# Kernel tuning notes

Hardware: AMD Instinct MI355X
Metric: run time of the kernel (lower is better)

## Reference

```python
import jax, jax.numpy as jnp
import numpy as np

KSIZE = 7
FEAT_SIZE = 64
BETA = 0.02


def _resize_bilinear_ac(x, out_h, out_w):
    """Bilinear resize with align_corners=True. x: (B, C, H, W)."""
    H, W = x.shape[-2], x.shape[-1]
    ys = jnp.linspace(0.0, H - 1.0, out_h)
    xs = jnp.linspace(0.0, W - 1.0, out_w)
    y0 = jnp.clip(jnp.floor(ys).astype(jnp.int32), 0, H - 1)
    x0 = jnp.clip(jnp.floor(xs).astype(jnp.int32), 0, W - 1)
    y1 = jnp.minimum(y0 + 1, H - 1)
    x1 = jnp.minimum(x0 + 1, W - 1)
    wy = (ys - y0.astype(x.dtype))[None, None, :, None]
    wx = (xs - x0.astype(x.dtype))[None, None, None, :]
    rows = x[:, :, y0, :] * (1.0 - wy) + x[:, :, y1, :] * wy      # (B,C,out_h,W)
    out = rows[:, :, :, x0] * (1.0 - wx) + rows[:, :, :, x1] * wx  # (B,C,out_h,out_w)
    return out


def _sce(feat, w, b):
    """EfficientSpatialContextNet: shifted local-correlation context + 1x1 conv + relu."""
    B, C, h, wd = feat.shape
    k, pad = KSIZE, KSIZE // 2
    # F.normalize(p=2, dim=1) with eps=1e-12 (clamped norm)
    fn = feat / jnp.maximum(jnp.sqrt(jnp.sum(feat * feat, axis=1, keepdims=True)), 1e-12)
    fp = jnp.pad(fn, ((0, 0), (0, 0), (pad, pad), (pad, pad)))
    offsets = ([(i, i) for i in range(k)]
               + [(i, pad) for i in range(k)]
               + [(i, k - 1 - i) for i in range(k)]
               + [(pad, i) for i in range(k)])
    ctx = jnp.stack([jnp.sum(fp[:, :, r:h + r, c:wd + c] * fn, axis=1)
                     for (r, c) in offsets], axis=1)  # (B, 4k, h, w)
    out = jnp.concatenate([feat, ctx], axis=1)        # (B, C+4k, h, w)
    out = jnp.einsum('oc,bchw->bohw', w, out) + b[None, :, None, None]
    return jax.nn.relu(out)


def _l2norm(f):
    # FeatureL2Norm: eps added inside sqrt
    return f / jnp.sqrt(jnp.sum(f * f, axis=1, keepdims=True) + 1e-6)


def _forward(src_feat, tgt_feat, sce_w, sce_b):
    fs = FEAT_SIZE
    s = _l2norm(_sce(src_feat, sce_w, sce_b))
    t = _l2norm(_sce(tgt_feat, sce_w, sce_b))
    B, C, hs, ws = s.shape
    ht, wt = t.shape[2], t.shape[3]
    Ls, Lt = hs * ws, ht * wt
    corr = jnp.einsum('bcs,bct->bst', s.reshape(B, C, Ls), t.reshape(B, C, Lt))
    # mutual NN filter (Rocco et al.)
    smax = jnp.max(corr, axis=2, keepdims=True)
    tmax = jnp.max(corr, axis=1, keepdims=True)
    smax = jnp.where(smax == 0, 1e-30, smax)
    tmax = jnp.where(tmax == 0, 1e-30, tmax)
    corr = corr * ((corr / smax) * (corr / tmax))
    # resize corr on source grid, then on target grid (bilinear, align_corners=True)
    c_s2t = jnp.transpose(corr, (0, 2, 1)).reshape(B, Lt, hs, ws)
    c_s2t = _resize_bilinear_ac(c_s2t, fs, fs)                       # (B, Lt, fs, fs)
    c_t2s = jnp.transpose(c_s2t.reshape(B, Lt, fs * fs), (0, 2, 1)).reshape(B, fs * fs, ht, wt)
    c = _resize_bilinear_ac(c_t2s, fs, fs)                           # (B, fs*fs, fs, fs)
    # soft argmax with temperature (softmax over source positions)
    p = jax.nn.softmax(c / BETA, axis=1).reshape(B, fs, fs, fs, fs)  # (B, hs', ws', ht', wt')
    xn = jnp.linspace(-1.0, 1.0, fs).astype(c.dtype)
    yn = jnp.linspace(-1.0, 1.0, fs).astype(c.dtype)
    grid_x = jnp.einsum('bijhw,j->bhw', p, xn)
    grid_y = jnp.einsum('bijhw,i->bhw', p, yn)
    flow_norm = jnp.stack([grid_x, grid_y], axis=1)                  # (B, 2, fs, fs)
    # unnormalise mapping and convert to flow
    H = W = fs
    mx = (flow_norm[:, 0] + 1.0) * (W - 1) / 2.0
    my = (flow_norm[:, 1] + 1.0) * (H - 1) / 2.0
    xx = jnp.arange(W, dtype=flow_norm.dtype)[None, None, :]
    yy = jnp.arange(H, dtype=flow_norm.dtype)[None, :, None]
    flow = jnp.stack([mx - xx, my - yy], axis=1)                     # (B, 2, fs, fs)
    return flow


def setup_inputs() -> dict:
    key = jax.random.key(0)
    k1, k2, k3 = jax.random.split(key, 3)
    B, C, h, w = 4, 1024, 32, 32
    src_feat = jax.random.normal(k1, (B, C, h, w), dtype=jnp.float32)
    tgt_feat = jax.random.normal(k2, (B, C, h, w), dtype=jnp.float32)
    sce_w = jax.random.normal(k3, (2048, C + 4 * KSIZE), dtype=jnp.float32) * 0.03
    sce_b = jnp.zeros((2048,), dtype=jnp.float32)
    return {"src_feat": src_feat, "tgt_feat": tgt_feat, "sce_w": sce_w, "sce_b": sce_b}


def reference(src_feat, tgt_feat, sce_w, sce_b):
    return _forward(src_feat, tgt_feat, sce_w, sce_b)
```

## Files before the change

### kernel.cpp

```cpp
#include <hip/hip_runtime.h>
#include <math.h>

#define HW    1024
#define CIN   1024
#define CCTX  28
#define CALL  1052
#define COUT  2048
#define CCHNK 512

typedef _Float16 half8   __attribute__((ext_vector_type(8)));
typedef _Float16 half4_t __attribute__((ext_vector_type(4)));
typedef float    f32x4   __attribute__((ext_vector_type(4)));

__device__ __forceinline__ void split_f16(float x, _Float16& h, _Float16& l) {
    _Float16 hh = (_Float16)x;
    h = hh;
    l = (_Float16)(x - (float)hh);
}
__device__ __forceinline__ float f4get(const float4& v, int e) {
    return e == 0 ? v.x : e == 1 ? v.y : e == 2 ? v.z : v.w;
}

__global__ void pnorm_kernel(const float* __restrict__ src, const float* __restrict__ tgt,
                             float* __restrict__ pnorm) {
    int img = blockIdx.x;
    int p = blockIdx.y * 64 + threadIdx.x;
    const float* feat = (img < 4) ? src + (size_t)img * CIN * HW
                                  : tgt + (size_t)(img - 4) * CIN * HW;
    float ss = 0.f;
    for (int c = 0; c < CIN; ++c) {
        float v = feat[(size_t)c * HW + p];
        ss = fmaf(v, v, ss);
    }
    pnorm[img * HW + p] = fmaxf(sqrtf(ss), 1e-12f);
}

__global__ void ctx_kernel(const float* __restrict__ src, const float* __restrict__ tgt,
                           const float* __restrict__ pnorm, float* __restrict__ ctx) {
    int img = blockIdx.x;
    int y = blockIdx.y;
    int tid = threadIdx.x;
    int o = tid >> 5;
    int x = tid & 31;
    const float* feat = (img < 4) ? src + (size_t)img * CIN * HW
                                  : tgt + (size_t)(img - 4) * CIN * HW;
    int g = o / 7, i = o % 7;
    int r, c;
    if (g == 0)      { r = i; c = i; }
    else if (g == 1) { r = i; c = 3; }
    else if (g == 2) { r = i; c = 6 - i; }
    else             { r = 3; c = i; }
    int y2 = y + r - 3, x2 = x + c - 3;
    int p = y * 32 + x;
    float outv = 0.f;
    if (y2 >= 0 && y2 < 32 && x2 >= 0 && x2 < 32) {
        int p2 = y2 * 32 + x2;
        const float* f0 = feat + p;
        const float* f1 = feat + p2;
        float acc = 0.f;
        for (int ch = 0; ch < CIN; ++ch)
            acc = fmaf(f0[(size_t)ch * HW], f1[(size_t)ch * HW], acc);
        outv = acc / (pnorm[img * HW + p] * pnorm[img * HW + p2]);
    }
    ctx[((size_t)img * CCTX + o) * HW + p] = outv;
}

template <bool FIRST>
__global__ __launch_bounds__(256, 2) void conv_mfma(
    const float* __restrict__ src, const float* __restrict__ tgt,
    const float* __restrict__ ctxb, const float* __restrict__ w,
    const float* __restrict__ bias, float* __restrict__ ychunk,
    float* __restrict__ nrm_parts, int c0) {
    __shared__ __align__(16) char smem[55296];
    _Float16* Ah = (_Float16*)smem;
    _Float16* Al = Ah + 64 * 72;
    _Float16* Bh = Al + 64 * 72;
    _Float16* Bl = Bh + 128 * 72;

    int cb = blockIdx.x;
    int pb = blockIdx.y;
    int img = blockIdx.z;
    int n0 = pb * 64;
    int m0g = c0 + cb * 128;
    const float* feat = (img < 4) ? src + (size_t)img * CIN * HW
                                  : tgt + (size_t)(img - 4) * CIN * HW;
    const float* ctxi = ctxb + (size_t)img * CCTX * HW;
    int tid = threadIdx.x;

    int aq = tid & 15, ar = tid >> 4;
    int brow = tid >> 1, bh_ = tid & 1;

    float4 xa[4], xb[8];
    auto loadA = [&](int k0) {
#pragma unroll
        for (int j = 0; j < 4; ++j) {
            int k = k0 + ar * 4 + j;
            if (k < CIN)       xa[j] = *(const float4*)(feat + (size_t)k * HW + n0 + aq * 4);
            else if (k < CALL) xa[j] = *(const float4*)(ctxi + (size_t)(k - CIN) * HW + n0 + aq * 4);
            else               xa[j] = make_float4(0.f, 0.f, 0.f, 0.f);
        }
    };
    auto loadB = [&](int k0) {
#pragma unroll
        for (int i = 0; i < 8; ++i) {
            int k = k0 + bh_ * 32 + i * 4;
            xb[i] = (k < CALL) ? *(const float4*)(w + (size_t)(m0g + brow) * CALL + k)
                               : make_float4(0.f, 0.f, 0.f, 0.f);
        }
    };
    auto storeLDS = [&]() {
#pragma unroll
        for (int p = 0; p < 4; ++p) {
            half4_t h, l;
#pragma unroll
            for (int j = 0; j < 4; ++j) {
                _Float16 hh, ll; split_f16(f4get(xa[j], p), hh, ll);
                h[j] = hh; l[j] = ll;
            }
            int row = aq * 4 + p;
            *(half4_t*)(Ah + row * 72 + ar * 4) = h;
            *(half4_t*)(Al + row * 72 + ar * 4) = l;
        }
#pragma unroll
        for (int g = 0; g < 4; ++g) {
            half8 h, l;
#pragma unroll
            for (int e = 0; e < 8; ++e) {
                _Float16 hh, ll; split_f16(f4get(xb[g * 2 + (e >> 2)], e & 3), hh, ll);
                h[e] = hh; l[e] = ll;
            }
            *(half8*)(Bh + brow * 72 + bh_ * 32 + g * 8) = h;
            *(half8*)(Bl + brow * 72 + bh_ * 32 + g * 8) = l;
        }
    };

    int lane = tid & 63, wv = tid >> 6;
    int wm = wv >> 1, wn = wv & 1;
    int frow = lane & 15;
    int kcol = (lane >> 4) * 8;

    f32x4 acc[2][4] = {};
    const int NT = 17;
    loadA(0); loadB(0); storeLDS();
    __syncthreads();
    for (int s = 0; s < NT; ++s) {
        if (s + 1 < NT) { loadA((s + 1) * 64); loadB((s + 1) * 64); }
#pragma unroll
        for (int ks = 0; ks < 2; ++ks) {
            int ko = ks * 32 + kcol;
            half8 ah[2], al_[2], bhv[4], blv[4];
#pragma unroll
            for (int fm = 0; fm < 2; ++fm) {
                int r = wm * 32 + fm * 16 + frow;
                ah[fm]  = *(const half8*)(Ah + r * 72 + ko);
                al_[fm] = *(const half8*)(Al + r * 72 + ko);
            }
#pragma unroll
            for (int fn = 0; fn < 4; ++fn) {
                int r = wn * 64 + fn * 16 + frow;
                bhv[fn] = *(const half8*)(Bh + r * 72 + ko);
                blv[fn] = *(const half8*)(Bl + r * 72 + ko);
            }
#pragma unroll
            for (int fm = 0; fm < 2; ++fm)
#pragma unroll
                for (int fn = 0; fn < 4; ++fn) {
                    acc[fm][fn] = __builtin_amdgcn_mfma_f32_16x16x32_f16(ah[fm],  bhv[fn], acc[fm][fn], 0, 0, 0);
                    acc[fm][fn] = __builtin_amdgcn_mfma_f32_16x16x32_f16(ah[fm],  blv[fn], acc[fm][fn], 0, 0, 0);
                    acc[fm][fn] = __builtin_amdgcn_mfma_f32_16x16x32_f16(al_[fm], bhv[fn], acc[fm][fn], 0, 0, 0);
                }
        }
        __syncthreads();
        if (s + 1 < NT) { storeLDS(); __syncthreads(); }
    }

    float* ybounce = (float*)smem;
    float* ns = ybounce + 64 * 132;
    float psum[2][4] = {};
#pragma unroll
    for (int fm = 0; fm < 2; ++fm)
#pragma unroll
        for (int fn = 0; fn < 4; ++fn) {
            int chan_l = wn * 64 + fn * 16 + (lane & 15);
            float bv = bias[m0g + chan_l];
#pragma unroll
            for (int r = 0; r < 4; ++r) {
                float v = fmaxf(acc[fm][fn][r] + bv, 0.f);
                int pix_l = wm * 32 + fm * 16 + (lane >> 4) * 4 + r;
                ybounce[pix_l * 132 + chan_l] = v;
                psum[fm][r] = fmaf(v, v, psum[fm][r]);
            }
        }
#pragma unroll
    for (int off = 1; off <= 8; off <<= 1)
#pragma unroll
        for (int fm = 0; fm < 2; ++fm)
#pragma unroll
            for (int r = 0; r < 4; ++r)
                psum[fm][r] = psum[fm][r] + __shfl_xor(psum[fm][r], off);
    if ((lane & 15) == 0) {
#pragma unroll
        for (int fm = 0; fm < 2; ++fm)
#pragma unroll
            for (int r = 0; r < 4; ++r)
                ns[wn * 64 + wm * 32 + fm * 16 + (lane >> 4) * 4 + r] = psum[fm][r];
    }
    __syncthreads();
    {
        int row = tid >> 2, seg = tid & 3;
        float* yp = ychunk + ((size_t)img * HW + n0 + row) * CCHNK + cb * 128 + seg * 32;
#pragma unroll
        for (int i = 0; i < 8; ++i)
            *(float4*)(yp + i * 4) = *(float4*)(ybounce + row * 132 + seg * 32 + i * 4);
    }
    if (tid < 64) {
        float sv = ns[tid] + ns[64 + tid];
        float* np = nrm_parts + ((size_t)img * 4 + cb) * HW + n0 + tid;
        if (FIRST) *np = sv; else *np += sv;
    }
}

template <int MODE>
__global__ __launch_bounds__(256, 2) void corr_mfma(
    const float* __restrict__ ychunk, const float* __restrict__ nrm_sq,
    float* __restrict__ corrT, float* __restrict__ spar, float* __restrict__ tpar) {
    __shared__ __align__(16) char smem[55296];
    _Float16* Ah = (_Float16*)smem;
    _Float16* Al = Ah + 64 * 72;
    _Float16* Bh = Al + 64 * 72;
    _Float16* Bl = Bh + 128 * 72;

    int sb = blockIdx.x, tb = blockIdx.y, b = blockIdx.z;
    int t0 = tb * 64, s0 = sb * 128;
    const float* ytg = ychunk + (size_t)(4 + b) * HW * CCHNK;
    const float* ysr = ychunk + (size_t)b * HW * CCHNK;
    int tid = threadIdx.x;
    int arow = tid >> 2, akq = tid & 3;
    int brow = tid >> 1, bh_ = tid & 1;

    float4 xa[4], xb[8];
    auto loadA = [&](int k0) {
#pragma unroll
        for (int i = 0; i < 4; ++i)
            xa[i] = *(const float4*)(ytg + (size_t)(t0 + arow) * CCHNK + k0 + akq * 16 + i * 4);
    };
    auto loadB = [&](int k0) {
#pragma unroll
        for (int i = 0; i < 8; ++i)
            xb[i] = *(const float4*)(ysr + (size_t)(s0 + brow) * CCHNK + k0 + bh_ * 32 + i * 4);
    };
    auto storeLDS = [&]() {
#pragma unroll
        for (int g = 0; g < 2; ++g) {
            half8 h, l;
#pragma unroll
            for (int e = 0; e < 8; ++e) {
                _Float16 hh, ll; split_f16(f4get(xa[g * 2 + (e >> 2)], e & 3), hh, ll);
                h[e] = hh; l[e] = ll;
            }
            *(half8*)(Ah + arow * 72 + akq * 16 + g * 8) = h;
            *(half8*)(Al + arow * 72 + akq * 16 + g * 8) = l;
        }
#pragma unroll
        for (int g = 0; g < 4; ++g) {
            half8 h, l;
#pragma unroll
            for (int e = 0; e < 8; ++e) {
                _Float16 hh, ll; split_f16(f4get(xb[g * 2 + (e >> 2)], e & 3), hh, ll);
                h[e] = hh; l[e] = ll;
            }
            *(half8*)(Bh + brow * 72 + bh_ * 32 + g * 8) = h;
            *(half8*)(Bl + brow * 72 + bh_ * 32 + g * 8) = l;
        }
    };

    int lane = tid & 63, wv = tid >> 6;
    int wm = wv >> 1, wn = wv & 1;
    int frow = lane & 15;
    int kcol = (lane >> 4) * 8;

    f32x4 acc[2][4] = {};
    const int NT = CCHNK / 64;
    loadA(0); loadB(0); storeLDS();
    __syncthreads();
    for (int s = 0; s < NT; ++s) {
        if (s + 1 < NT) { loadA((s + 1) * 64); loadB((s + 1) * 64); }
#pragma unroll
        for (int ks = 0; ks < 2; ++ks) {
            int ko = ks * 32 + kcol;
            half8 ah[2], al_[2], bhv[4], blv[4];
#pragma unroll
            for (int fm = 0; fm < 2; ++fm) {
                int r = wm * 32 + fm * 16 + frow;
                ah[fm]  = *(const half8*)(Ah + r * 72 + ko);
                al_[fm] = *(const half8*)(Al + r * 72 + ko);
            }
#pragma unroll
            for (int fn = 0; fn < 4; ++fn) {
                int r = wn * 64 + fn * 16 + frow;
                bhv[fn] = *(const half8*)(Bh + r * 72 + ko);
                blv[fn] = *(const half8*)(Bl + r * 72 + ko);
            }
#pragma unroll
            for (int fm = 0; fm < 2; ++fm)
#pragma unroll
                for (int fn = 0; fn < 4; ++fn) {
                    acc[fm][fn] = __builtin_amdgcn_mfma_f32_16x16x32_f16(ah[fm],  bhv[fn], acc[fm][fn], 0, 0, 0);
                    acc[fm][fn] = __builtin_amdgcn_mfma_f32_16x16x32_f16(ah[fm],  blv[fn], acc[fm][fn], 0, 0, 0);
                    acc[fm][fn] = __builtin_amdgcn_mfma_f32_16x16x32_f16(al_[fm], bhv[fn], acc[fm][fn], 0, 0, 0);
                }
        }
        __syncthreads();
        if (s + 1 < NT) { storeLDS(); __syncthreads(); }
    }

    float rnt[2][4], rns[4];
    float rowmax[2][4] = {};
    float colmax[4] = {};
    if (MODE == 2) {
#pragma unroll
        for (int fm = 0; fm < 2; ++fm)
#pragma unroll
            for (int r = 0; r < 4; ++r) {
                int t = t0 + wm * 32 + fm * 16 + (lane >> 4) * 4 + r;
                rnt[fm][r] = 1.f / sqrtf(nrm_sq[(size_t)(4 + b) * HW + t] + 1e-6f);
            }
#pragma unroll
        for (int fn = 0; fn < 4; ++fn) {
            int s_ = s0 + wn * 64 + fn * 16 + (lane & 15);
            rns[fn] = 1.f / sqrtf(nrm_sq[(size_t)b * HW + s_] + 1e-6f);
        }
    }
#pragma unroll
    for (int fm = 0; fm < 2; ++fm)
#pragma unroll
        for (int r = 0; r < 4; ++r) {
            int t = t0 + wm * 32 + fm * 16 + (lane >> 4) * 4 + r;
            float* cp = corrT + ((size_t)b * HW + t) * HW + s0 + wn * 64 + (lane & 15);
#pragma unroll
            for (int fn = 0; fn < 4; ++fn) {
                float v = acc[fm][fn][r];
                if (MODE >= 1) v += cp[fn * 16];
                if (MODE == 2) {
                    v *= rnt[fm][r] * rns[fn];
                    rowmax[fm][r] = fmaxf(rowmax[fm][r], v);
                    colmax[fn] = fmaxf(colmax[fn], v);
                }
                cp[fn * 16] = v;
            }
        }
    if (MODE == 2) {
        float* rm = (float*)smem;
        float* cm = rm + 128;
#pragma unroll
        for (int off = 1; off <= 8; off <<= 1)
#pragma unroll
            for (int fm = 0; fm < 2; ++fm)
#pragma unroll
                for (int r = 0; r < 4; ++r)
                    rowmax[fm][r] = fmaxf(rowmax[fm][r], __shfl_xor(rowmax[fm][r], off));
        if ((lane & 15) == 0) {
#pragma unroll
            for (int fm = 0; fm < 2; ++fm)
#pragma unroll
                for (int r = 0; r < 4; ++r)
                    rm[wn * 64 + wm * 32 + fm * 16 + (lane >> 4) * 4 + r] = rowmax[fm][r];
        }
#pragma unroll
        for (int off = 16; off <= 32; off <<= 1)
#pragma unroll
            for (int fn = 0; fn < 4; ++fn)
                colmax[fn] = fmaxf(colmax[fn], __shfl_xor(colmax[fn], off));
        if ((lane >> 4) == 0) {
#pragma unroll
            for (int fn = 0; fn < 4; ++fn)
                cm[wv * 64 + fn * 16 + (lane & 15)] = colmax[fn];
        }
        __syncthreads();
        if (tid < 64)
            tpar[((size_t)b * 8 + sb) * HW + t0 + tid] = fmaxf(rm[tid], rm[64 + tid]);
        if (tid < 128) {
            int q = tid >> 6;
            float mv = fmaxf(cm[q * 64 + (tid & 63)], cm[(2 + q) * 64 + (tid & 63)]);
            spar[((size_t)b * 16 + tb) * HW + s0 + tid] = mv;
        }
    }
}

__global__ void nrm_reduce(const float* __restrict__ nrm_parts, float* __restrict__ nrm_sq) {
    int img = blockIdx.y;
    int p = blockIdx.x * 256 + threadIdx.x;
    float s = 0.f;
#pragma unroll
    for (int mb = 0; mb < 4; ++mb)
        s += nrm_parts[((size_t)img * 4 + mb) * HW + p];
    nrm_sq[img * HW + p] = s;
}

__global__ void combine_max(const float* __restrict__ spar, const float* __restrict__ tpar,
                            float* __restrict__ smax, float* __restrict__ tmax) {
    int b = blockIdx.y;
    int i = blockIdx.x * 256 + threadIdx.x;
    float m = 0.f;
#pragma unroll
    for (int q = 0; q < 16; ++q) m = fmaxf(m, spar[((size_t)b * 16 + q) * HW + i]);
    smax[b * HW + i] = m;
    float m2 = 0.f;
#pragma unroll
    for (int q = 0; q < 8; ++q) m2 = fmaxf(m2, tpar[((size_t)b * 8 + q) * HW + i]);
    tmax[b * HW + i] = m2;
}

__global__ __launch_bounds__(256) void final_kernel(const float* __restrict__ corrT,
                                                    const float* __restrict__ smax,
                                                    const float* __restrict__ tmax,
                                                    float* __restrict__ out) {
    __shared__ float vsh[1024];
    __shared__ float rbuf[16];
    int b = blockIdx.z;
    int typ = blockIdx.y;
    int txp = blockIdx.x;
    int tid = threadIdx.x;

    float fy = typ * (31.0f / 63.0f);
    int y0 = min((int)fy, 31); int y1 = min(y0 + 1, 31);
    float wy = fy - (float)y0;
    float fx = txp * (31.0f / 63.0f);
    int x0 = min((int)fx, 31); int x1 = min(x0 + 1, 31);
    float wx = fx - (float)x0;
    int tA = y0 * 32 + x0, tB = y0 * 32 + x1, tC = y1 * 32 + x0, tD = y1 * 32 + x1;
    const float* base = corrT + (size_t)b * HW * HW;
    const float* rA = base + (size_t)tA * HW;
    const float* rB = base + (size_t)tB * HW;
    const float* rC = base + (size_t)tC * HW;
    const float* rD = base + (size_t)tD * HW;
    float tmA_ = tmax[b * HW + tA]; if (tmA_ == 0.f) tmA_ = 1e-30f;
    float tmB_ = tmax[b * HW + tB]; if (tmB_ == 0.f) tmB_ = 1e-30f;
    float tmC_ = tmax[b * HW + tC]; if (tmC_ == 0.f) tmC_ = 1e-30f;
    float tmD_ = tmax[b * HW + tD]; if (tmD_ == 0.f) tmD_ = 1e-30f;
    float itA = 1.f / tmA_, itB = 1.f / tmB_, itC = 1.f / tmC_, itD = 1.f / tmD_;
    float wA = (1.f - wy) * (1.f - wx), wB = (1.f - wy) * wx;
    float wC = wy * (1.f - wx), wD = wy * wx;
#pragma unroll
    for (int u = 0; u < 4; ++u) {
        int s = u * 256 + tid;
        float sm = smax[b * HW + s]; if (sm == 0.f) sm = 1e-30f;
        float is = 1.f / sm;
        float a = rA[s]; a = a * a * a * is * itA;
        float b2 = rB[s]; b2 = b2 * b2 * b2 * is * itB;
        float c2 = rC[s]; c2 = c2 * c2 * c2 * is * itC;
        float d2 = rD[s]; d2 = d2 * d2 * d2 * is * itD;
        vsh[s] = wA * a + wB * b2 + wC * c2 + wD * d2;
    }
    __syncthreads();

    float cv[16];
    float lmax = -1e30f;
#pragma unroll
    for (int u = 0; u < 16; ++u) {
        int sp = u * 256 + tid;
        int i = sp >> 6, j = sp & 63;
        float gy = i * (31.0f / 63.0f);
        int sy0 = min((int)gy, 31); int sy1 = min(sy0 + 1, 31);
        float wyy = gy - (float)sy0;
        float gx = j * (31.0f / 63.0f);
        int sx0 = min((int)gx, 31); int sx1 = min(sx0 + 1, 31);
        float wxx = gx - (float)sx0;
        float v00 = vsh[sy0 * 32 + sx0], v01 = vsh[sy0 * 32 + sx1];
        float v10 = vsh[sy1 * 32 + sx0], v11 = vsh[sy1 * 32 + sx1];
        float c = (v00 * (1.f - wxx) + v01 * wxx) * (1.f - wyy)
                + (v10 * (1.f - wxx) + v11 * wxx) * wyy;
        cv[u] = c * 50.0f;
        lmax = fmaxf(lmax, cv[u]);
    }
#pragma unroll
    for (int off = 32; off >= 1; off >>= 1) lmax = fmaxf(lmax, __shfl_down(lmax, off));
    int lane = tid & 63, wv = tid >> 6;
    if (lane == 0) rbuf[wv] = lmax;
    __syncthreads();
    if (tid == 0) {
        float m = rbuf[0];
        for (int i = 1; i < 4; ++i) m = fmaxf(m, rbuf[i]);
        rbuf[0] = m;
    }
    __syncthreads();
    float m = rbuf[0];

    float e0 = 0.f, ex = 0.f, ey = 0.f;
#pragma unroll
    for (int u = 0; u < 16; ++u) {
        int sp = u * 256 + tid;
        int i = sp >> 6, j = sp & 63;
        float e = __expf(cv[u] - m);
        e0 += e;
        ex = fmaf(e, j * (2.0f / 63.0f) - 1.0f, ex);
        ey = fmaf(e, i * (2.0f / 63.0f) - 1.0f, ey);
    }
#pragma unroll
    for (int off = 32; off >= 1; off >>= 1) {
        e0 += __shfl_down(e0, off);
        ex += __shfl_down(ex, off);
        ey += __shfl_down(ey, off);
    }
    if (lane == 0) { rbuf[4 + wv] = e0; rbuf[8 + wv] = ex; rbuf[12 + wv] = ey; }
    __syncthreads();
    if (tid == 0) {
        float s0 = rbuf[4] + rbuf[5] + rbuf[6] + rbuf[7];
        float sx = rbuf[8] + rbuf[9] + rbuf[10] + rbuf[11];
        float sy = rbuf[12] + rbuf[13] + rbuf[14] + rbuf[15];
        float gx = sx / s0, gy = sy / s0;
        float mx = (gx + 1.f) * 31.5f;
        float my = (gy + 1.f) * 31.5f;
        out[(((size_t)b * 2 + 0) * 64 + typ) * 64 + txp] = mx - (float)txp;
        out[(((size_t)b * 2 + 1) * 64 + typ) * 64 + txp] = my - (float)typ;
    }
}

extern "C" void kernel_launch(void* const* d_in, const int* in_sizes, int n_in,
                              void* d_out, int out_size, void* d_ws, size_t ws_size,
                              hipStream_t stream) {
    const float* src  = (const float*)d_in[0];
    const float* tgt  = (const float*)d_in[1];
    const float* sw   = (const float*)d_in[2];
    const float* sb   = (const float*)d_in[3];
    float* out = (float*)d_out;

    float* corrT      = (float*)d_ws;
    float* nrm_parts  = corrT + 4194304;
    float* tpar       = nrm_parts + 32768;
    float* nrm_sq     = nrm_parts + 65536;
    float* smax       = nrm_sq + 8192;
    float* spar       = smax + 4096;
    float* tmax       = spar + 65536;
    float* pnorm      = tmax + 4096;
    float* ctxbuf     = pnorm + 8192;
    float* ychunk     = ctxbuf + 229376;

    pnorm_kernel<<<dim3(8, 16), 64, 0, stream>>>(src, tgt, pnorm);
    ctx_kernel<<<dim3(8, 32), 896, 0, stream>>>(src, tgt, pnorm, ctxbuf);

    conv_mfma<true><<<dim3(4, 16, 8), 256, 0, stream>>>(src, tgt, ctxbuf, sw, sb,
                                                        ychunk, nrm_parts, 0);
    corr_mfma<0><<<dim3(8, 16, 4), 256, 0, stream>>>(ychunk, nrm_sq, corrT, spar, tpar);
    for (int c = 1; c < 3; ++c) {
        conv_mfma<false><<<dim3(4, 16, 8), 256, 0, stream>>>(src, tgt, ctxbuf, sw, sb,
                                                             ychunk, nrm_parts, c * CCHNK);
        corr_mfma<1><<<dim3(8, 16, 4), 256, 0, stream>>>(ychunk, nrm_sq, corrT, spar, tpar);
    }
    conv_mfma<false><<<dim3(4, 16, 8), 256, 0, stream>>>(src, tgt, ctxbuf, sw, sb,
                                                         ychunk, nrm_parts, 3 * CCHNK);
    nrm_reduce<<<dim3(4, 8), 256, 0, stream>>>(nrm_parts, nrm_sq);
    corr_mfma<2><<<dim3(8, 16, 4), 256, 0, stream>>>(ychunk, nrm_sq, corrT, spar, tpar);

    combine_max<<<dim3(4, 4), 256, 0, stream>>>(spar, tpar, smax, tmax);
    final_kernel<<<dim3(64, 64, 4), 256, 0, stream>>>(corrT, smax, tmax, out);
}
```

Measured before the change: 598.4 us.

## Double-buffer LDS in conv/corr GEMMs, cheaper fp16 split, split pnorm reduction

The conv and corr MFMA kernels move from a single-buffered 64-wide K tile to a double-buffered 32-wide K tile, which removes one barrier per iteration and lets the LDS store of the next tile overlap the current compute. The hi/lo fp16 split now masks mantissa bits and uses packed cvt_pkrtz conversions instead of scalar casts. The pnorm reduction is split across four channel partitions plus a combine kernel for more parallelism. The ctx and pnorm loops are unrolled with multiple accumulators, and the final kernel hoists per-column interpolation math. Smaller K tiles mean more loop iterations, and the new split changes rounding slightly.

```diff
diff --git a/kernel.cpp b/kernel.cpp
--- a/kernel.cpp
+++ b/kernel.cpp
@@ -10,29 +10,52 @@
 
 typedef _Float16 half8   __attribute__((ext_vector_type(8)));
 typedef _Float16 half4_t __attribute__((ext_vector_type(4)));
+typedef _Float16 half2_t __attribute__((ext_vector_type(2)));
+typedef __fp16   fp16x2  __attribute__((ext_vector_type(2)));
 typedef float    f32x4   __attribute__((ext_vector_type(4)));
 
-__device__ __forceinline__ void split_f16(float x, _Float16& h, _Float16& l) {
-    _Float16 hh = (_Float16)x;
-    h = hh;
-    l = (_Float16)(x - (float)hh);
+__device__ __forceinline__ void split2(float a0, float a1, half2_t& h, half2_t& l) {
+    float h0 = __uint_as_float(__float_as_uint(a0) & 0xFFFFE000u);
+    float h1 = __uint_as_float(__float_as_uint(a1) & 0xFFFFE000u);
+    fp16x2 hp = __builtin_amdgcn_cvt_pkrtz(h0, h1);
+    fp16x2 lp = __builtin_amdgcn_cvt_pkrtz(a0 - h0, a1 - h1);
+    h = __builtin_bit_cast(half2_t, hp);
+    l = __builtin_bit_cast(half2_t, lp);
+}
+__device__ __forceinline__ void split4(float4 v, half4_t& h, half4_t& l) {
+    half2_t ha, la, hb, lb;
+    split2(v.x, v.y, ha, la);
+    split2(v.z, v.w, hb, lb);
+    h = __builtin_shufflevector(ha, hb, 0, 1, 2, 3);
+    l = __builtin_shufflevector(la, lb, 0, 1, 2, 3);
 }
 __device__ __forceinline__ float f4get(const float4& v, int e) {
     return e == 0 ? v.x : e == 1 ? v.y : e == 2 ? v.z : v.w;
 }
 
-__global__ void pnorm_kernel(const float* __restrict__ src, const float* __restrict__ tgt,
-                             float* __restrict__ pnorm) {
+__global__ void pnorm_part(const float* __restrict__ src, const float* __restrict__ tgt,
+                           float* __restrict__ parts) {
+    int img = blockIdx.x, pb = blockIdx.y, part = blockIdx.z;
+    int p = pb * 64 + threadIdx.x;
+    const float* feat = ((img < 4) ? src + (size_t)img * CIN * HW
+                                   : tgt + (size_t)(img - 4) * CIN * HW)
+                        + (size_t)part * 256 * HW + p;
+    float a4[4] = {};
+    for (int c = 0; c < 256; c += 8) {
+        float v[8];
+#pragma unroll
+        for (int j = 0; j < 8; ++j) v[j] = feat[(size_t)(c + j) * HW];
+#pragma unroll
+        for (int j = 0; j < 8; ++j) a4[j & 3] = fmaf(v[j], v[j], a4[j & 3]);
+    }
+    parts[(size_t)part * 8192 + img * 1024 + p] = (a4[0] + a4[1]) + (a4[2] + a4[3]);
+}
+__global__ void pnorm_combine(const float* __restrict__ parts, float* __restrict__ pnorm) {
     int img = blockIdx.x;
     int p = blockIdx.y * 64 + threadIdx.x;
-    const float* feat = (img < 4) ? src + (size_t)img * CIN * HW
-                                  : tgt + (size_t)(img - 4) * CIN * HW;
-    float ss = 0.f;
-    for (int c = 0; c < CIN; ++c) {
-        float v = feat[(size_t)c * HW + p];
-        ss = fmaf(v, v, ss);
-    }
-    pnorm[img * HW + p] = fmaxf(sqrtf(ss), 1e-12f);
+    float s = parts[img * 1024 + p] + parts[8192 + img * 1024 + p]
+            + parts[16384 + img * 1024 + p] + parts[24576 + img * 1024 + p];
+    pnorm[img * HW + p] = fmaxf(sqrtf(s), 1e-12f);
 }
 
 __global__ void ctx_kernel(const float* __restrict__ src, const float* __restrict__ tgt,
@@ -57,44 +80,48 @@
         int p2 = y2 * 32 + x2;
         const float* f0 = feat + p;
         const float* f1 = feat + p2;
-        float acc = 0.f;
-        for (int ch = 0; ch < CIN; ++ch)
-            acc = fmaf(f0[(size_t)ch * HW], f1[(size_t)ch * HW], acc);
+        float a4[4] = {};
+        for (int ch = 0; ch < CIN; ch += 8) {
+            float va[8], vb[8];
+#pragma unroll
+            for (int j = 0; j < 8; ++j) {
+                va[j] = f0[(size_t)(ch + j) * HW];
+                vb[j] = f1[(size_t)(ch + j) * HW];
+            }
+#pragma unroll
+            for (int j = 0; j < 8; ++j) a4[j & 3] = fmaf(va[j], vb[j], a4[j & 3]);
+        }
+        float acc = (a4[0] + a4[1]) + (a4[2] + a4[3]);
         outv = acc / (pnorm[img * HW + p] * pnorm[img * HW + p2]);
     }
     ctx[((size_t)img * CCTX + o) * HW + p] = outv;
 }
 
+#define ABUF_H 2560
+#define BBUF_H 5120
+#define BUF_H  15360
 template <bool FIRST>
 __global__ __launch_bounds__(256, 2) void conv_mfma(
     const float* __restrict__ src, const float* __restrict__ tgt,
     const float* __restrict__ ctxb, const float* __restrict__ w,
     const float* __restrict__ bias, float* __restrict__ ychunk,
     float* __restrict__ nrm_parts, int c0) {
-    __shared__ __align__(16) char smem[55296];
-    _Float16* Ah = (_Float16*)smem;
-    _Float16* Al = Ah + 64 * 72;
-    _Float16* Bh = Al + 64 * 72;
-    _Float16* Bl = Bh + 128 * 72;
-
-    int cb = blockIdx.x;
-    int pb = blockIdx.y;
-    int img = blockIdx.z;
-    int n0 = pb * 64;
-    int m0g = c0 + cb * 128;
+    __shared__ __align__(16) _Float16 lds[2 * BUF_H];
+
+    int cb = blockIdx.x, pb = blockIdx.y, img = blockIdx.z;
+    int n0 = pb * 64, m0g = c0 + cb * 128;
     const float* feat = (img < 4) ? src + (size_t)img * CIN * HW
                                   : tgt + (size_t)(img - 4) * CIN * HW;
     const float* ctxi = ctxb + (size_t)img * CCTX * HW;
     int tid = threadIdx.x;
-
     int aq = tid & 15, ar = tid >> 4;
     int brow = tid >> 1, bh_ = tid & 1;
 
-    float4 xa[4], xb[8];
+    float4 xa[2], xb[4];
     auto loadA = [&](int k0) {
 #pragma unroll
-        for (int j = 0; j < 4; ++j) {
-            int k = k0 + ar * 4 + j;
+        for (int j = 0; j < 2; ++j) {
+            int k = k0 + ar * 2 + j;
             if (k < CIN)       xa[j] = *(const float4*)(feat + (size_t)k * HW + n0 + aq * 4);
             else if (k < CALL) xa[j] = *(const float4*)(ctxi + (size_t)(k - CIN) * HW + n0 + aq * 4);
             else               xa[j] = make_float4(0.f, 0.f, 0.f, 0.f);
@@ -102,79 +129,74 @@
     };
     auto loadB = [&](int k0) {
 #pragma unroll
-        for (int i = 0; i < 8; ++i) {
-            int k = k0 + bh_ * 32 + i * 4;
+        for (int i = 0; i < 4; ++i) {
+            int k = k0 + bh_ * 16 + i * 4;
             xb[i] = (k < CALL) ? *(const float4*)(w + (size_t)(m0g + brow) * CALL + k)
                                : make_float4(0.f, 0.f, 0.f, 0.f);
         }
     };
-    auto storeLDS = [&]() {
+    auto storeLDS = [&](int b) {
+        _Float16* Ah = lds + b * BUF_H;
+        _Float16* Al = Ah + ABUF_H;
+        _Float16* Bh = Al + ABUF_H;
+        _Float16* Bl = Bh + BBUF_H;
 #pragma unroll
         for (int p = 0; p < 4; ++p) {
+            half2_t h, l;
+            split2(f4get(xa[0], p), f4get(xa[1], p), h, l);
+            int row = aq * 4 + p;
+            *(half2_t*)(Ah + row * 40 + ar * 2) = h;
+            *(half2_t*)(Al + row * 40 + ar * 2) = l;
+        }
+#pragma unroll
+        for (int i = 0; i < 4; ++i) {
             half4_t h, l;
-#pragma unroll
-            for (int j = 0; j < 4; ++j) {
-                _Float16 hh, ll; split_f16(f4get(xa[j], p), hh, ll);
-                h[j] = hh; l[j] = ll;
+            split4(xb[i], h, l);
+            *(half4_t*)(Bh + brow * 40 + bh_ * 16 + i * 4) = h;
+            *(half4_t*)(Bl + brow * 40 + bh_ * 16 + i * 4) = l;
+        }
+    };
+
+    int lane = tid & 63, wv4 = tid >> 6;
+    int wm = wv4 >> 1, wn = wv4 & 1;
+    int frow = lane & 15, kcol = (lane >> 4) * 8;
+
+    f32x4 acc[2][4] = {};
+    const int NT = 33;
+    loadA(0); loadB(0); storeLDS(0);
+    __syncthreads();
+    for (int t = 0; t < NT; ++t) {
+        if (t + 1 < NT) { loadA((t + 1) * 32); loadB((t + 1) * 32); }
+        const _Float16* Ah = lds + (t & 1) * BUF_H;
+        const _Float16* Al = Ah + ABUF_H;
+        const _Float16* Bh = Al + ABUF_H;
+        const _Float16* Bl = Bh + BBUF_H;
+        half8 ah[2], alr[2], bhr[4], blr[4];
+#pragma unroll
+        for (int fm = 0; fm < 2; ++fm) {
+            int r = wm * 32 + fm * 16 + frow;
+            ah[fm]  = *(const half8*)(Ah + r * 40 + kcol);
+            alr[fm] = *(const half8*)(Al + r * 40 + kcol);
+        }
+#pragma unroll
+        for (int fn = 0; fn < 4; ++fn) {
+            int r = wn * 64 + fn * 16 + frow;
+            bhr[fn] = *(const half8*)(Bh + r * 40 + kcol);
+            blr[fn] = *(const half8*)(Bl + r * 40 + kcol);
+        }
+#pragma unroll
+        for (int fm = 0; fm < 2; ++fm)
+#pragma unroll
+            for (int fn = 0; fn < 4; ++fn) {
+                acc[fm][fn] = __builtin_amdgcn_mfma_f32_16x16x32_f16(ah[fm],  bhr[fn], acc[fm][fn], 0, 0, 0);
+                acc[fm][fn] = __builtin_amdgcn_mfma_f32_16x16x32_f16(ah[fm],  blr[fn], acc[fm][fn], 0, 0, 0);
+                acc[fm][fn] = __builtin_amdgcn_mfma_f32_16x16x32_f16(alr[fm], bhr[fn], acc[fm][fn], 0, 0, 0);
             }
-            int row = aq * 4 + p;
-            *(half4_t*)(Ah + row * 72 + ar * 4) = h;
-            *(half4_t*)(Al + row * 72 + ar * 4) = l;
-        }
-#pragma unroll
-        for (int g = 0; g < 4; ++g) {
-            half8 h, l;
-#pragma unroll
-            for (int e = 0; e < 8; ++e) {
-                _Float16 hh, ll; split_f16(f4get(xb[g * 2 + (e >> 2)], e & 3), hh, ll);
-                h[e] = hh; l[e] = ll;
-            }
-            *(half8*)(Bh + brow * 72 + bh_ * 32 + g * 8) = h;
-            *(half8*)(Bl + brow * 72 + bh_ * 32 + g * 8) = l;
-        }
-    };
-
-    int lane = tid & 63, wv = tid >> 6;
-    int wm = wv >> 1, wn = wv & 1;
-    int frow = lane & 15;
-    int kcol = (lane >> 4) * 8;
-
-    f32x4 acc[2][4] = {};
-    const int NT = 17;
-    loadA(0); loadB(0); storeLDS();
-    __syncthreads();
-    for (int s = 0; s < NT; ++s) {
-        if (s + 1 < NT) { loadA((s + 1) * 64); loadB((s + 1) * 64); }
-#pragma unroll
-        for (int ks = 0; ks < 2; ++ks) {
-            int ko = ks * 32 + kcol;
-            half8 ah[2], al_[2], bhv[4], blv[4];
-#pragma unroll
-            for (int fm = 0; fm < 2; ++fm) {
-                int r = wm * 32 + fm * 16 + frow;
-                ah[fm]  = *(const half8*)(Ah + r * 72 + ko);
-                al_[fm] = *(const half8*)(Al + r * 72 + ko);
-            }
-#pragma unroll
-            for (int fn = 0; fn < 4; ++fn) {
-                int r = wn * 64 + fn * 16 + frow;
-                bhv[fn] = *(const half8*)(Bh + r * 72 + ko);
-                blv[fn] = *(const half8*)(Bl + r * 72 + ko);
-            }
-#pragma unroll
-            for (int fm = 0; fm < 2; ++fm)
-#pragma unroll
-                for (int fn = 0; fn < 4; ++fn) {
-                    acc[fm][fn] = __builtin_amdgcn_mfma_f32_16x16x32_f16(ah[fm],  bhv[fn], acc[fm][fn], 0, 0, 0);
-                    acc[fm][fn] = __builtin_amdgcn_mfma_f32_16x16x32_f16(ah[fm],  blv[fn], acc[fm][fn], 0, 0, 0);
-                    acc[fm][fn] = __builtin_amdgcn_mfma_f32_16x16x32_f16(al_[fm], bhv[fn], acc[fm][fn], 0, 0, 0);
-                }
-        }
+        if (t + 1 < NT) storeLDS((t + 1) & 1);
         __syncthreads();
-        if (s + 1 < NT) { storeLDS(); __syncthreads(); }
-    }
-
-    float* ybounce = (float*)smem;
+    }
+
+    float* ybounce = (float*)lds;
     float* ns = ybounce + 64 * 132;
     float psum[2][4] = {};
 #pragma unroll
@@ -224,11 +246,7 @@
 __global__ __launch_bounds__(256, 2) void corr_mfma(
     const float* __restrict__ ychunk, const float* __restrict__ nrm_sq,
     float* __restrict__ corrT, float* __restrict__ spar, float* __restrict__ tpar) {
-    __shared__ __align__(16) char smem[55296];
-    _Float16* Ah = (_Float16*)smem;
-    _Float16* Al = Ah + 64 * 72;
-    _Float16* Bh = Al + 64 * 72;
-    _Float16* Bl = Bh + 128 * 72;
+    __shared__ __align__(16) _Float16 lds[2 * BUF_H];
 
     int sb = blockIdx.x, tb = blockIdx.y, b = blockIdx.z;
     int t0 = tb * 64, s0 = sb * 128;
@@ -238,80 +256,73 @@
     int arow = tid >> 2, akq = tid & 3;
     int brow = tid >> 1, bh_ = tid & 1;
 
-    float4 xa[4], xb[8];
-    auto loadA = [&](int k0) {
+    float4 xa[2], xb[4];
+    auto loadAB = [&](int k0) {
+#pragma unroll
+        for (int i = 0; i < 2; ++i)
+            xa[i] = *(const float4*)(ytg + (size_t)(t0 + arow) * CCHNK + k0 + akq * 8 + i * 4);
 #pragma unroll
         for (int i = 0; i < 4; ++i)
-            xa[i] = *(const float4*)(ytg + (size_t)(t0 + arow) * CCHNK + k0 + akq * 16 + i * 4);
+            xb[i] = *(const float4*)(ysr + (size_t)(s0 + brow) * CCHNK + k0 + bh_ * 16 + i * 4);
     };
-    auto loadB = [&](int k0) {
-#pragma unroll
-        for (int i = 0; i < 8; ++i)
-            xb[i] = *(const float4*)(ysr + (size_t)(s0 + brow) * CCHNK + k0 + bh_ * 32 + i * 4);
+    auto storeLDS = [&](int bb) {
+        _Float16* Ah = lds + bb * BUF_H;
+        _Float16* Al = Ah + ABUF_H;
+        _Float16* Bh = Al + ABUF_H;
+        _Float16* Bl = Bh + BBUF_H;
+#pragma unroll
+        for (int i = 0; i < 2; ++i) {
+            half4_t h, l;
+            split4(xa[i], h, l);
+            *(half4_t*)(Ah + arow * 40 + akq * 8 + i * 4) = h;
+            *(half4_t*)(Al + arow * 40 + akq * 8 + i * 4) = l;
+        }
+#pragma unroll
+        for (int i = 0; i < 4; ++i) {
+            half4_t h, l;
+            split4(xb[i], h, l);
+            *(half4_t*)(Bh + brow * 40 + bh_ * 16 + i * 4) = h;
+            *(half4_t*)(Bl + brow * 40 + bh_ * 16 + i * 4) = l;
+        }
     };
-    auto storeLDS = [&]() {
-#pragma unroll
-        for (int g = 0; g < 2; ++g) {
-            half8 h, l;
-#pragma unroll
-            for (int e = 0; e < 8; ++e) {
-                _Float16 hh, ll; split_f16(f4get(xa[g * 2 + (e >> 2)], e & 3), hh, ll);
-                h[e] = hh; l[e] = ll;
+
+    int lane = tid & 63, wv4 = tid >> 6;
+    int wm = wv4 >> 1, wn = wv4 & 1;
+    int frow = lane & 15, kcol = (lane >> 4) * 8;
+
+    f32x4 acc[2][4] = {};
+    const int NT = CCHNK / 32;
+    loadAB(0); storeLDS(0);
+    __syncthreads();
+    for (int t = 0; t < NT; ++t) {
+        if (t + 1 < NT) loadAB((t + 1) * 32);
+        const _Float16* Ah = lds + (t & 1) * BUF_H;
+        const _Float16* Al = Ah + ABUF_H;
+        const _Float16* Bh = Al + ABUF_H;
+        const _Float16* Bl = Bh + BBUF_H;
+        half8 ah[2], alr[2], bhr[4], blr[4];
+#pragma unroll
+        for (int fm = 0; fm < 2; ++fm) {
+            int r = wm * 32 + fm * 16 + frow;
+            ah[fm]  = *(const half8*)(Ah + r * 40 + kcol);
+            alr[fm] = *(const half8*)(Al + r * 40 + kcol);
+        }
+#pragma unroll
+        for (int fn = 0; fn < 4; ++fn) {
+            int r = wn * 64 + fn * 16 + frow;
+            bhr[fn] = *(const half8*)(Bh + r * 40 + kcol);
+            blr[fn] = *(const half8*)(Bl + r * 40 + kcol);
+        }
+#pragma unroll
+        for (int fm = 0; fm < 2; ++fm)
+#pragma unroll
+            for (int fn = 0; fn < 4; ++fn) {
+                acc[fm][fn] = __builtin_amdgcn_mfma_f32_16x16x32_f16(ah[fm],  bhr[fn], acc[fm][fn], 0, 0, 0);
+                acc[fm][fn] = __builtin_amdgcn_mfma_f32_16x16x32_f16(ah[fm],  blr[fn], acc[fm][fn], 0, 0, 0);
+                acc[fm][fn] = __builtin_amdgcn_mfma_f32_16x16x32_f16(alr[fm], bhr[fn], acc[fm][fn], 0, 0, 0);
             }
-            *(half8*)(Ah + arow * 72 + akq * 16 + g * 8) = h;
-            *(half8*)(Al + arow * 72 + akq * 16 + g * 8) = l;
-        }
-#pragma unroll
-        for (int g = 0; g < 4; ++g) {
-            half8 h, l;
-#pragma unroll
-            for (int e = 0; e < 8; ++e) {
-                _Float16 hh, ll; split_f16(f4get(xb[g * 2 + (e >> 2)], e & 3), hh, ll);
-                h[e] = hh; l[e] = ll;
-            }
-            *(half8*)(Bh + brow * 72 + bh_ * 32 + g * 8) = h;
-            *(half8*)(Bl + brow * 72 + bh_ * 32 + g * 8) = l;
-        }
-    };
-
-    int lane = tid & 63, wv = tid >> 6;
-    int wm = wv >> 1, wn = wv & 1;
-    int frow = lane & 15;
-    int kcol = (lane >> 4) * 8;
-
-    f32x4 acc[2][4] = {};
-    const int NT = CCHNK / 64;
-    loadA(0); loadB(0); storeLDS();
-    __syncthreads();
-    for (int s = 0; s < NT; ++s) {
-        if (s + 1 < NT) { loadA((s + 1) * 64); loadB((s + 1) * 64); }
-#pragma unroll
-        for (int ks = 0; ks < 2; ++ks) {
-            int ko = ks * 32 + kcol;
-            half8 ah[2], al_[2], bhv[4], blv[4];
-#pragma unroll
-            for (int fm = 0; fm < 2; ++fm) {
-                int r = wm * 32 + fm * 16 + frow;
-                ah[fm]  = *(const half8*)(Ah + r * 72 + ko);
-                al_[fm] = *(const half8*)(Al + r * 72 + ko);
-            }
-#pragma unroll
-            for (int fn = 0; fn < 4; ++fn) {
-                int r = wn * 64 + fn * 16 + frow;
-                bhv[fn] = *(const half8*)(Bh + r * 72 + ko);
-                blv[fn] = *(const half8*)(Bl + r * 72 + ko);
-            }
-#pragma unroll
-            for (int fm = 0; fm < 2; ++fm)
-#pragma unroll
-                for (int fn = 0; fn < 4; ++fn) {
-                    acc[fm][fn] = __builtin_amdgcn_mfma_f32_16x16x32_f16(ah[fm],  bhv[fn], acc[fm][fn], 0, 0, 0);
-                    acc[fm][fn] = __builtin_amdgcn_mfma_f32_16x16x32_f16(ah[fm],  blv[fn], acc[fm][fn], 0, 0, 0);
-                    acc[fm][fn] = __builtin_amdgcn_mfma_f32_16x16x32_f16(al_[fm], bhv[fn], acc[fm][fn], 0, 0, 0);
-                }
-        }
+        if (t + 1 < NT) storeLDS((t + 1) & 1);
         __syncthreads();
-        if (s + 1 < NT) { storeLDS(); __syncthreads(); }
     }
 
     float rnt[2][4], rns[4];
@@ -350,7 +361,7 @@
             }
         }
     if (MODE == 2) {
-        float* rm = (float*)smem;
+        float* rm = (float*)lds;
         float* cm = rm + 128;
 #pragma unroll
         for (int off = 1; off <= 8; off <<= 1)
@@ -374,7 +385,7 @@
         if ((lane >> 4) == 0) {
 #pragma unroll
             for (int fn = 0; fn < 4; ++fn)
-                cm[wv * 64 + fn * 16 + (lane & 15)] = colmax[fn];
+                cm[wv4 * 64 + fn * 16 + (lane & 15)] = colmax[fn];
         }
         __syncthreads();
         if (tid < 64)
@@ -454,29 +465,30 @@
     }
     __syncthreads();
 
+    int jx = tid & 63;
+    int wvq = tid >> 6;
+    float gxx = jx * (31.0f / 63.0f);
+    int sx0 = min((int)gxx, 31), sx1 = min(sx0 + 1, 31);
+    float wxx = gxx - (float)sx0, iwxx = 1.f - wxx;
+    float xnj = jx * (2.0f / 63.0f) - 1.0f;
+
     float cv[16];
     float lmax = -1e30f;
 #pragma unroll
     for (int u = 0; u < 16; ++u) {
-        int sp = u * 256 + tid;
-        int i = sp >> 6, j = sp & 63;
-        float gy = i * (31.0f / 63.0f);
-        int sy0 = min((int)gy, 31); int sy1 = min(sy0 + 1, 31);
+        int iy = u * 4 + wvq;
+        float gy = iy * (31.0f / 63.0f);
+        int sy0 = min((int)gy, 31), sy1 = min(sy0 + 1, 31);
         float wyy = gy - (float)sy0;
-        float gx = j * (31.0f / 63.0f);
-        int sx0 = min((int)gx, 31); int sx1 = min(sx0 + 1, 31);
-        float wxx = gx - (float)sx0;
-        float v00 = vsh[sy0 * 32 + sx0], v01 = vsh[sy0 * 32 + sx1];
-        float v10 = vsh[sy1 * 32 + sx0], v11 = vsh[sy1 * 32 + sx1];
-        float c = (v00 * (1.f - wxx) + v01 * wxx) * (1.f - wyy)
-                + (v10 * (1.f - wxx) + v11 * wxx) * wyy;
-        cv[u] = c * 50.0f;
+        float r0 = vsh[sy0 * 32 + sx0] * iwxx + vsh[sy0 * 32 + sx1] * wxx;
+        float r1 = vsh[sy1 * 32 + sx0] * iwxx + vsh[sy1 * 32 + sx1] * wxx;
+        cv[u] = (r0 * (1.f - wyy) + r1 * wyy) * 50.0f;
         lmax = fmaxf(lmax, cv[u]);
     }
 #pragma unroll
     for (int off = 32; off >= 1; off >>= 1) lmax = fmaxf(lmax, __shfl_down(lmax, off));
-    int lane = tid & 63, wv = tid >> 6;
-    if (lane == 0) rbuf[wv] = lmax;
+    int lane = tid & 63;
+    if (lane == 0) rbuf[wvq] = lmax;
     __syncthreads();
     if (tid == 0) {
         float m = rbuf[0];
@@ -489,12 +501,11 @@
     float e0 = 0.f, ex = 0.f, ey = 0.f;
 #pragma unroll
     for (int u = 0; u < 16; ++u) {
-        int sp = u * 256 + tid;
-        int i = sp >> 6, j = sp & 63;
+        int iy = u * 4 + wvq;
         float e = __expf(cv[u] - m);
         e0 += e;
-        ex = fmaf(e, j * (2.0f / 63.0f) - 1.0f, ex);
-        ey = fmaf(e, i * (2.0f / 63.0f) - 1.0f, ey);
+        ex = fmaf(e, xnj, ex);
+        ey = fmaf(e, iy * (2.0f / 63.0f) - 1.0f, ey);
     }
 #pragma unroll
     for (int off = 32; off >= 1; off >>= 1) {
@@ -502,7 +513,7 @@
         ex += __shfl_down(ex, off);
         ey += __shfl_down(ey, off);
     }
-    if (lane == 0) { rbuf[4 + wv] = e0; rbuf[8 + wv] = ex; rbuf[12 + wv] = ey; }
+    if (lane == 0) { rbuf[4 + wvq] = e0; rbuf[8 + wvq] = ex; rbuf[12 + wvq] = ey; }
     __syncthreads();
     if (tid == 0) {
         float s0 = rbuf[4] + rbuf[5] + rbuf[6] + rbuf[7];
@@ -535,8 +546,10 @@
     float* pnorm      = tmax + 4096;
     float* ctxbuf     = pnorm + 8192;
     float* ychunk     = ctxbuf + 229376;
-
-    pnorm_kernel<<<dim3(8, 16), 64, 0, stream>>>(src, tgt, pnorm);
+    float* pparts     = ychunk;
+
+    pnorm_part<<<dim3(8, 16, 4), 64, 0, stream>>>(src, tgt, pparts);
+    pnorm_combine<<<dim3(8, 16), 64, 0, stream>>>(pparts, pnorm);
     ctx_kernel<<<dim3(8, 32), 896, 0, stream>>>(src, tgt, pnorm, ctxbuf);
 
     conv_mfma<true><<<dim3(4, 16, 8), 256, 0, stream>>>(src, tgt, ctxbuf, sw, sb,
```

After: 531.3 us. 1.13x faster.
